# Performance work log

Hardware: AMD Instinct MI355X
Metric: run time of the kernel (lower is better)

Reference implementation:

```python
import jax, jax.numpy as jnp
import numpy as np

HEAD_DIM = 32
KERNEL = 9
DILATION = 3


def setup_inputs() -> dict:
    key = jax.random.key(0)
    k1, k2, k3 = jax.random.split(key, 3)
    B, d, L = 4, 512, 4096
    q = jax.random.normal(k1, (B, d, 1, L), dtype=jnp.float32)
    k = jax.random.normal(k2, (B, d, 1, L), dtype=jnp.float32)
    v = jax.random.normal(k3, (B, d, 1, L), dtype=jnp.float32)
    return {"q": q, "k": k, "v": v}


def reference(q, k, v):
    # q,k,v: [B, d, 1, L]; output: [B, 1, L, d]
    B, d, _, N = q.shape
    hd = HEAD_DIM
    h = d // hd
    K = KERNEL
    dil = DILATION
    pad = dil * (K - 1) // 2
    scale = hd ** -0.5

    # Window gather indices replicating nn.Unfold with zero padding.
    idx = jnp.arange(N)[:, None] + jnp.arange(K)[None, :] * dil - pad  # [N, K]
    valid = ((idx >= 0) & (idx < N)).astype(q.dtype)                   # [N, K]
    idxc = jnp.clip(idx, 0, N - 1)

    qr = q.reshape(B, h, hd, N)
    kr = k.reshape(B, h, hd, N)
    vr = v.reshape(B, h, hd, N)

    # Unfolded windows: [B, h, hd, N, K], zero outside bounds (like Unfold padding)
    kw = kr[:, :, :, idxc] * valid
    vw = vr[:, :, :, idxc] * valid

    attn = jnp.einsum('bhdn,bhdnk->bhnk', qr, kw) * scale
    attn = jax.nn.softmax(attn, axis=-1)
    out = jnp.einsum('bhnk,bhdnk->bhnd', attn, vw)  # [B, h, N, hd]
    # torch: transpose(1,2).reshape(B,1,N,d) -> heads concatenated per token
    return out.transpose(0, 2, 1, 3).reshape(B, 1, N, d)
```

## Files before the change

kernel.cpp:

```cpp
#include <hip/hip_runtime.h>
#include <math.h>

#define NPOS 4096
#define DCH  512
#define HD   32
#define NH   16
#define KW   9
#define DIL  3
#define PAD  12
#define TILE   32
#define NTILES (NPOS / TILE)
#define SPANT  (TILE + 2*PAD)
#define RS     60
#define ROWC   (RS / 4)
#define KCHK   (HD * ROWC)
#define KINST  8
#define CSPL   8
#define CPT    (HD / CSPL)
#define TPT    4
#define WSPAN  28
#define WCHK   (WSPAN / 4)
#define NXCD   8

typedef float floatx4 __attribute__((ext_vector_type(4)));

__device__ __forceinline__ void gload16(const float* g, float* l) {
    __builtin_amdgcn_global_load_lds(
        (const __attribute__((address_space(1))) void*)g,
        (__attribute__((address_space(3))) void*)l,
        16, 0, 0);
}

__device__ __forceinline__ float dpp_sum8(float x) {
    int t;
    t = __builtin_amdgcn_update_dpp(0, __float_as_int(x), 0xB1, 0xF, 0xF, true);
    x += __int_as_float(t);
    t = __builtin_amdgcn_update_dpp(0, __float_as_int(x), 0x4E, 0xF, 0xF, true);
    x += __int_as_float(t);
    t = __builtin_amdgcn_update_dpp(0, __float_as_int(x), 0x141, 0xF, 0xF, true);
    x += __int_as_float(t);
    return x;
}

__device__ __forceinline__ void vload_row(const float* row, int w0, float* w) {
#pragma unroll
    for (int u = 0; u < WCHK; ++u) {
        int g0 = min(max(w0 + 4 * u, 0), NPOS - 4);
        float4 x = *(const float4*)(row + g0);
        w[4*u] = x.x; w[4*u+1] = x.y; w[4*u+2] = x.z; w[4*u+3] = x.w;
    }
}

__global__ __launch_bounds__(64) void dilate_attn_kernel(
    const float* __restrict__ q,
    const float* __restrict__ k,
    const float* __restrict__ v,
    float* __restrict__ out)
{
    __shared__ float ks[HD * RS];

    const int id   = blockIdx.x;
    const int xcd  = id & (NXCD - 1);
    const int seq  = id >> 3;
    const int tile = seq & (NTILES - 1);
    const int bh   = ((seq >> 7) << 3) | xcd;

    const int n0t  = tile * TILE;
    const int ws   = n0t - PAD;

    const size_t cb = (size_t)bh * HD * NPOS;
    const float* qg = q + cb;
    const float* kg = k + cb;
    const float* vg = v + cb;

    const int tid = threadIdx.x;
    const int cs  = tid & (CSPL - 1);
    const int lg  = tid >> 3;
    const int n0  = n0t + lg * TPT;
    const int w0  = n0 - PAD;

    const float scale = 0.17677669529663687f;

    float4 qv[CPT];
#pragma unroll
    for (int i = 0; i < CPT; ++i)
        qv[i] = *(const float4*)(qg + (size_t)(cs * CPT + i) * NPOS + n0);
    asm volatile("" ::: "memory");

#pragma unroll
    for (int it = 0; it < KINST; ++it) {
        int c = it * 64 + tid;
        if (c < KCHK) {
            int row = c / ROWC;
            int c4  = c - row * ROWC;
            int g0  = min(max(ws + c4 * 4, 0), NPOS - 4);
            gload16(kg + (size_t)row * NPOS + g0, &ks[c * 4]);
        }
    }
    asm volatile("" ::: "memory");

    float w[WSPAN];
    vload_row(vg + (size_t)(cs * CPT + 0) * NPOS, w0, w);

    asm volatile("s_waitcnt vmcnt(7)" ::: "memory");

    float s[TPT][KW];
#pragma unroll
    for (int t = 0; t < TPT; ++t)
#pragma unroll
        for (int j = 0; j < KW; ++j) s[t][j] = 0.0f;

#pragma unroll
    for (int i = 0; i < CPT; ++i) {
        int row = cs * CPT + i;
        float kw[WSPAN];
        const float4* wp = (const float4*)&ks[row * RS + lg * TPT];
#pragma unroll
        for (int u = 0; u < WCHK; ++u) {
            float4 x = wp[u];
            kw[4*u] = x.x; kw[4*u+1] = x.y; kw[4*u+2] = x.z; kw[4*u+3] = x.w;
        }
        float qt[TPT] = {qv[i].x, qv[i].y, qv[i].z, qv[i].w};
#pragma unroll
        for (int t = 0; t < TPT; ++t)
#pragma unroll
            for (int j = 0; j < KW; ++j)
                s[t][j] = fmaf(qt[t], kw[t + 3*j], s[t][j]);
    }

#pragma unroll
    for (int t = 0; t < TPT; ++t)
#pragma unroll
        for (int j = 0; j < KW; ++j)
            s[t][j] = dpp_sum8(s[t][j]);

    const bool masked = (tile == 0) || (tile == NTILES - 1);
    if (!masked) {
#pragma unroll
        for (int t = 0; t < TPT; ++t) {
            float m = -INFINITY;
#pragma unroll
            for (int j = 0; j < KW; ++j) {
                float x = s[t][j] * scale;
                s[t][j] = x;
                m = fmaxf(m, x);
            }
            float sum = 0.0f;
#pragma unroll
            for (int j = 0; j < KW; ++j) {
                float e = __expf(s[t][j] - m);
                s[t][j] = e;
                sum += e;
            }
            float inv = 1.0f / sum;
#pragma unroll
            for (int j = 0; j < KW; ++j) s[t][j] *= inv;
        }
    } else {
#pragma unroll
        for (int t = 0; t < TPT; ++t) {
            float vm[KW];
            float m = -INFINITY;
#pragma unroll
            for (int j = 0; j < KW; ++j) {
                vm[j] = ((unsigned)(n0 + t + 3*j - PAD) < NPOS) ? 1.0f : 0.0f;
                float x = s[t][j] * scale * vm[j];
                s[t][j] = x;
                m = fmaxf(m, x);
            }
            float sum = 0.0f;
#pragma unroll
            for (int j = 0; j < KW; ++j) {
                float e = __expf(s[t][j] - m);
                s[t][j] = e;
                sum += e;
            }
            float inv = 1.0f / sum;
#pragma unroll
            for (int j = 0; j < KW; ++j)
                s[t][j] *= inv * vm[j];
        }
    }

    float o[TPT][CPT];
#pragma unroll
    for (int t = 0; t < TPT; ++t)
#pragma unroll
        for (int i = 0; i < CPT; ++i) o[t][i] = 0.0f;

#pragma unroll
    for (int i = 0; i < CPT; ++i) {
#pragma unroll
        for (int t = 0; t < TPT; ++t)
#pragma unroll
            for (int j = 0; j < KW; ++j)
                o[t][i] = fmaf(s[t][j], w[t + 3*j], o[t][i]);
        if (i < CPT - 1)
            vload_row(vg + (size_t)(cs * CPT + i + 1) * NPOS, w0, w);
    }

    const int b  = bh >> 4;
    const int hh = bh & (NH - 1);
#pragma unroll
    for (int t = 0; t < TPT; ++t) {
        float* op = out + ((size_t)(b * NPOS + n0 + t)) * DCH + hh * HD + cs * CPT;
        floatx4 val = {o[t][0], o[t][1], o[t][2], o[t][3]};
        __builtin_nontemporal_store(val, (floatx4*)op);
    }
}

extern "C" void kernel_launch(void* const* d_in, const int* in_sizes, int n_in,
                              void* d_out, int out_size, void* d_ws, size_t ws_size,
                              hipStream_t stream) {
    const float* q = (const float*)d_in[0];
    const float* k = (const float*)d_in[1];
    const float* v = (const float*)d_in[2];
    float* out = (float*)d_out;

    const int grid = 4 * NH * NTILES;
    hipLaunchKernelGGL(dilate_attn_kernel, dim3(grid), dim3(64), 0, stream,
                       q, k, v, out);
}
```

Measured before the change: 142.4 us.

## Stage V tile through LDS with async global_load_lds reusing K buffer

```diff
diff --git a/kernel.cpp b/kernel.cpp
--- a/kernel.cpp
+++ b/kernel.cpp
@@ -42,15 +42,6 @@
     return x;
 }
 
-__device__ __forceinline__ void vload_row(const float* row, int w0, float* w) {
-#pragma unroll
-    for (int u = 0; u < WCHK; ++u) {
-        int g0 = min(max(w0 + 4 * u, 0), NPOS - 4);
-        float4 x = *(const float4*)(row + g0);
-        w[4*u] = x.x; w[4*u+1] = x.y; w[4*u+2] = x.z; w[4*u+3] = x.w;
-    }
-}
-
 __global__ __launch_bounds__(64) void dilate_attn_kernel(
     const float* __restrict__ q,
     const float* __restrict__ k,
@@ -77,9 +68,16 @@
     const int cs  = tid & (CSPL - 1);
     const int lg  = tid >> 3;
     const int n0  = n0t + lg * TPT;
-    const int w0  = n0 - PAD;
 
     const float scale = 0.17677669529663687f;
+
+    int crow[KINST], cg0[KINST];
+#pragma unroll
+    for (int it = 0; it < KINST; ++it) {
+        int c    = it * 64 + tid;
+        crow[it] = c / ROWC;
+        cg0[it]  = min(max(ws + (c - crow[it] * ROWC) * 4, 0), NPOS - 4);
+    }
 
     float4 qv[CPT];
 #pragma unroll
@@ -90,19 +88,11 @@
 #pragma unroll
     for (int it = 0; it < KINST; ++it) {
         int c = it * 64 + tid;
-        if (c < KCHK) {
-            int row = c / ROWC;
-            int c4  = c - row * ROWC;
-            int g0  = min(max(ws + c4 * 4, 0), NPOS - 4);
-            gload16(kg + (size_t)row * NPOS + g0, &ks[c * 4]);
-        }
-    }
-    asm volatile("" ::: "memory");
-
-    float w[WSPAN];
-    vload_row(vg + (size_t)(cs * CPT + 0) * NPOS, w0, w);
-
-    asm volatile("s_waitcnt vmcnt(7)" ::: "memory");
+        if (c < KCHK)
+            gload16(kg + (size_t)crow[it] * NPOS + cg0[it], &ks[c * 4]);
+    }
+
+    asm volatile("s_waitcnt vmcnt(0)" ::: "memory");
 
     float s[TPT][KW];
 #pragma unroll
@@ -113,19 +103,29 @@
 #pragma unroll
     for (int i = 0; i < CPT; ++i) {
         int row = cs * CPT + i;
-        float kw[WSPAN];
+        float w[WSPAN];
         const float4* wp = (const float4*)&ks[row * RS + lg * TPT];
 #pragma unroll
         for (int u = 0; u < WCHK; ++u) {
             float4 x = wp[u];
-            kw[4*u] = x.x; kw[4*u+1] = x.y; kw[4*u+2] = x.z; kw[4*u+3] = x.w;
+            w[4*u] = x.x; w[4*u+1] = x.y; w[4*u+2] = x.z; w[4*u+3] = x.w;
         }
         float qt[TPT] = {qv[i].x, qv[i].y, qv[i].z, qv[i].w};
 #pragma unroll
         for (int t = 0; t < TPT; ++t)
 #pragma unroll
             for (int j = 0; j < KW; ++j)
-                s[t][j] = fmaf(qt[t], kw[t + 3*j], s[t][j]);
+                s[t][j] = fmaf(qt[t], w[t + 3*j], s[t][j]);
+    }
+
+    asm volatile("s_waitcnt lgkmcnt(0)" ::: "memory");
+    __builtin_amdgcn_sched_barrier(0);
+
+#pragma unroll
+    for (int it = 0; it < KINST; ++it) {
+        int c = it * 64 + tid;
+        if (c < KCHK)
+            gload16(vg + (size_t)crow[it] * NPOS + cg0[it], &ks[c * 4]);
     }
 
 #pragma unroll
@@ -182,6 +182,8 @@
         }
     }
 
+    asm volatile("s_waitcnt vmcnt(0)" ::: "memory");
+
     float o[TPT][CPT];
 #pragma unroll
     for (int t = 0; t < TPT; ++t)
@@ -190,13 +192,19 @@
 
 #pragma unroll
     for (int i = 0; i < CPT; ++i) {
+        int row = cs * CPT + i;
+        float w[WSPAN];
+        const float4* wp = (const float4*)&ks[row * RS + lg * TPT];
+#pragma unroll
+        for (int u = 0; u < WCHK; ++u) {
+            float4 x = wp[u];
+            w[4*u] = x.x; w[4*u+1] = x.y; w[4*u+2] = x.z; w[4*u+3] = x.w;
+        }
 #pragma unroll
         for (int t = 0; t < TPT; ++t)
 #pragma unroll
             for (int j = 0; j < KW; ++j)
                 o[t][i] = fmaf(s[t][j], w[t + 3*j], o[t][i]);
-        if (i < CPT - 1)
-            vload_row(vg + (size_t)(cs * CPT + i + 1) * NPOS, w0, w);
     }
 
     const int b  = bh >> 4;
```

New measurement: 131.9 us. 1.08x faster.
